# Kernel optimization log

Measured on AMD Instinct MI355X. Metric: run time of the kernel, lower is better.

Reference implementation:

```python
import jax, jax.numpy as jnp
import numpy as np


def setup_inputs() -> dict:
    key = jax.random.key(0)
    ks = jax.random.split(key, 6)
    B, N, D, E, S, H = 4, 4096, 768, 4, 1024, 3072
    sc = lambda d: 1.0 / np.sqrt(d)
    return {
        "x": jax.random.normal(ks[0], (B, N, D), dtype=jnp.float32),
        "phi": jax.random.normal(ks[1], (E, S, D), dtype=jnp.float32) * sc(D),
        "w1": jax.random.normal(ks[2], (E, D, H), dtype=jnp.float32) * sc(D),
        "b1": jnp.zeros((E, H), dtype=jnp.float32),
        "w2": jax.random.normal(ks[3], (E, H, D), dtype=jnp.float32) * sc(H),
        "b2": jnp.zeros((E, D), dtype=jnp.float32),
    }


def reference(x, phi, w1, b1, w2, b2):
    # x: [B,N,D], phi: [E,S,D]
    logits = jnp.einsum('bnd,esd->bnes', x, phi)          # [B,N,E,S]
    B, N, E, S = logits.shape
    dispatch = jax.nn.softmax(logits, axis=1)             # softmax over tokens
    combine = jax.nn.softmax(
        logits.reshape(B, N, E * S), axis=-1
    ).reshape(B, N, E, S)                                 # softmax over all slots
    slots = jnp.einsum('bnd,bnes->besd', x, dispatch)     # [B,E,S,D]
    h = jax.nn.gelu(jnp.einsum('besd,edh->besh', slots, w1) + b1[None, :, None, :])
    y = jnp.einsum('besh,ehd->besd', h, w2) + b2[None, :, None, :]
    out = jnp.einsum('besd,bnes->bnd', y, combine)        # [B,N,D]
    return out
```

## Files before the change

kernel.cpp:

```cpp
#include <hip/hip_runtime.h>
#include <hip/hip_bf16.h>

using u16 = unsigned short;
using short8 = __attribute__((ext_vector_type(8))) short;
using floatx4 = __attribute__((ext_vector_type(4))) float;

#define DEVI static __device__ __forceinline__

constexpr int cB = 4, cN = 4096, cD = 768, cE = 4, cS = 1024, cH = 3072;
constexpr int cES = cE * cS;
constexpr int cHC = cH / 2;

DEVI u16 f2bf(float f) {
  union { float f; unsigned u; } v; v.f = f;
  unsigned r = v.u + 0x7fffu + ((v.u >> 16) & 1u);
  return (u16)(r >> 16);
}
DEVI float bf2f(u16 b) {
  union { unsigned u; float f; } v; v.u = ((unsigned)b) << 16;
  return v.f;
}
DEVI float gelu_tanh(float x) {
  float z = 1.5957691216057308f * (x + 0.044715f * x * x * x);
  z = fminf(fmaxf(z, -30.f), 30.f);
  float e = __expf(z);
  float t = (e - 1.f) / (e + 1.f);
  return 0.5f * x * (1.f + t);
}

DEVI void glds16(const u16* g, u16* l) {
  __builtin_amdgcn_global_load_lds(
      (const __attribute__((address_space(1))) void*)g,
      (__attribute__((address_space(3))) void*)l, 16, 0, 0);
}

__global__ __launch_bounds__(256) void zero_kernel(float* __restrict__ p, int n) {
  int i = blockIdx.x * 256 + threadIdx.x;
  if (i < n) p[i] = 0.f;
}

__global__ __launch_bounds__(256) void convert_kernel(const float* __restrict__ in,
                                                      u16* __restrict__ out, long n) {
  long stride = (long)gridDim.x * 256 * 4;
  for (long idx = ((long)blockIdx.x * 256 + threadIdx.x) * 4; idx < n; idx += stride) {
    float4 v = *(const float4*)(in + idx);
    ushort4 o;
    o.x = f2bf(v.x); o.y = f2bf(v.y); o.z = f2bf(v.z); o.w = f2bf(v.w);
    *(ushort4*)(out + idx) = o;
  }
}

DEVI u16 to_bf(float f) { return f2bf(f); }
DEVI u16 to_bf(u16 u) { return u; }

template <typename Tin>
__global__ __launch_bounds__(256) void transpose_bf16_kernel(const Tin* __restrict__ in,
                                                             u16* __restrict__ out,
                                                             int R, int C,
                                                             long strideIn, long strideOut) {
  __shared__ u16 tile[64][65];
  const Tin* inb = in + (long)blockIdx.z * strideIn;
  u16* outb = out + (long)blockIdx.z * strideOut;
  const int r0 = blockIdx.y * 64, c0 = blockIdx.x * 64;
  const int tid = threadIdx.x;
#pragma unroll
  for (int i = 0; i < 16; i++) {
    int idx = i * 256 + tid;
    int r = idx >> 6, c = idx & 63;
    tile[r][c] = to_bf(inb[(long)(r0 + r) * C + (c0 + c)]);
  }
  __syncthreads();
#pragma unroll
  for (int i = 0; i < 16; i++) {
    int idx = i * 256 + tid;
    int r = idx >> 6, c = idx & 63;
    outb[(long)(c0 + r) * R + (r0 + c)] = tile[c][r];
  }
}

__global__ __launch_bounds__(256) void rowsum_kernel(const u16* __restrict__ P,
                                                     float* __restrict__ Z, int cols) {
  long base = (long)blockIdx.x * cols;
  int tid = threadIdx.x;
  float s = 0.f;
  for (int c = tid * 4; c < cols; c += 256 * 4) {
    ushort4 v = *(const ushort4*)(P + base + c);
    s += bf2f(v.x) + bf2f(v.y) + bf2f(v.z) + bf2f(v.w);
  }
  for (int o = 32; o > 0; o >>= 1) s += __shfl_down(s, o, 64);
  __shared__ float ws4[4];
  if ((tid & 63) == 0) ws4[tid >> 6] = s;
  __syncthreads();
  if (tid == 0) Z[blockIdx.x] = ws4[0] + ws4[1] + ws4[2] + ws4[3];
}

__global__ __launch_bounds__(256) void colsum_kernel(const u16* __restrict__ P,
                                                     float* __restrict__ Z, int cols) {
  int col = blockIdx.x * 256 + threadIdx.x;
  int r0 = blockIdx.y * 256;
  float s = 0.f;
  for (int r = r0; r < r0 + 256; r++) s += bf2f(P[(long)r * cols + col]);
  atomicAdd(Z + col, s);
}

template <int EPI>
__global__ __launch_bounds__(256, 2) void gemm_nt(const u16* __restrict__ A,
                                                  const u16* __restrict__ Bm,
                                                  void* __restrict__ Cout,
                                                  int M, int Nn, int K,
                                                  long ldA, long ldB, long ldC,
                                                  long strideA, long strideB, int modB,
                                                  long strideC,
                                                  const float* __restrict__ epiVec,
                                                  long epiStride, int epiMod) {
  __shared__ u16 lds[4 * 8192];

  const int gx = gridDim.x;
  const int nwg = gx * gridDim.y;
  int flat = blockIdx.y * gx + blockIdx.x;
  if ((nwg & 7) == 0) flat = (flat & 7) * (nwg >> 3) + (flat >> 3);
  const int bxs = flat % gx, bys = flat / gx;

  const int bz = blockIdx.z;
  const u16* Ab = A + (long)bz * strideA;
  const u16* Bb = Bm + (long)(bz % modB) * strideB;
  const float* ev = epiVec + (long)(bz % epiMod) * epiStride;
  const int tileM = bys * 128, tileN = bxs * 128;
  const int tid = threadIdx.x;
  const int wave = tid >> 6, lane = tid & 63;
  const int quad = lane >> 4, l16 = lane & 15;
  const int wm = (wave >> 1) * 64, wn = (wave & 1) * 64;

  const int swzk = (((lane & 3) ^ ((lane >> 3) & 3)) << 3);
  const int r0 = wave * 32 + (lane >> 2);
  const u16* aG0 = Ab + (long)(tileM + r0) * ldA + swzk;
  const u16* aG1 = Ab + (long)(tileM + r0 + 16) * ldA + swzk;
  const u16* bG0 = Bb + (long)(tileN + r0) * ldB + swzk;
  const u16* bG1 = Bb + (long)(tileN + r0 + 16) * ldB + swzk;
  const int ldsW = wave * 1024;

  const int NT = K >> 5;

  auto STAGE = [&](int tt) {
    u16* l = &lds[(tt & 3) * 8192];
    const long ko = (long)tt << 5;
    glds16(aG0 + ko, l + ldsW);
    glds16(aG1 + ko, l + ldsW + 512);
    glds16(bG0 + ko, l + 4096 + ldsW);
    glds16(bG1 + ko, l + 4096 + ldsW + 512);
  };

  floatx4 acc[4][4] = {};
  const int sread = ((quad ^ ((l16 >> 1) & 3)) << 3);

  STAGE(0);
  if (NT > 1) STAGE(1);
  if (NT > 2) STAGE(2);

  for (int t = 0; t < NT; t++) {
    asm volatile("s_barrier" ::: "memory");
    if (t + 3 < NT) STAGE(t + 3);
    const int ahead = NT - 1 - t;
    if (ahead >= 3)      asm volatile("s_waitcnt vmcnt(12)" ::: "memory");
    else if (ahead == 2) asm volatile("s_waitcnt vmcnt(8)" ::: "memory");
    else if (ahead == 1) asm volatile("s_waitcnt vmcnt(4)" ::: "memory");
    else                 asm volatile("s_waitcnt vmcnt(0)" ::: "memory");
    asm volatile("s_barrier" ::: "memory");

    const u16* As = &lds[(t & 3) * 8192];
    const u16* Bs = As + 4096;
    short8 af[4], bq[4];
#pragma unroll
    for (int i = 0; i < 4; i++)
      af[i] = *(const short8*)&As[(wm + i * 16 + l16) * 32 + sread];
#pragma unroll
    for (int j = 0; j < 4; j++)
      bq[j] = *(const short8*)&Bs[(wn + j * 16 + l16) * 32 + sread];
    __builtin_amdgcn_s_setprio(1);
#pragma unroll
    for (int i = 0; i < 4; i++)
#pragma unroll
      for (int j = 0; j < 4; j++)
        acc[i][j] = __builtin_amdgcn_mfma_f32_16x16x32_bf16(af[i], bq[j], acc[i][j], 0, 0, 0);
    __builtin_amdgcn_s_setprio(0);
  }

  const long cBase = (long)bz * strideC;
#pragma unroll
  for (int i = 0; i < 4; i++) {
#pragma unroll
    for (int r = 0; r < 4; r++) {
      const int row = tileM + wm + i * 16 + quad * 4 + r;
      float rscale = 1.f;
      if (EPI == 1 || EPI == 4) rscale = 1.f / ev[row];
#pragma unroll
      for (int j = 0; j < 4; j++) {
        const int col = tileN + wn + j * 16 + l16;
        float v = acc[i][j][r];
        const long cIdx = cBase + (long)row * ldC + col;
        if (EPI == 0) v = __expf(v);
        if (EPI == 1 || EPI == 4) v *= rscale;
        if (EPI == 2) v = gelu_tanh(v + ev[col]);
        if (EPI == 3) v = v + ev[col];
        if (EPI == 5) v = v + bf2f(((u16*)Cout)[cIdx]);
        if (EPI == 4)
          ((float*)Cout)[cIdx] = v;
        else
          ((u16*)Cout)[cIdx] = f2bf(v);
      }
    }
  }
}

template <int EPI>
__global__ __launch_bounds__(512, 2) void gemm256(const u16* __restrict__ A,
                                                  const u16* __restrict__ Bm,
                                                  void* __restrict__ Cout,
                                                  int M, int Nn, int K,
                                                  long ldA, long ldB, long ldC,
                                                  long strideA, long strideB, int modB,
                                                  long strideC,
                                                  const float* __restrict__ epiVec,
                                                  long epiStride, int epiMod) {
  __shared__ u16 lds[2][2][2][8192];

  const int gx = gridDim.x;
  const int nwg = gx * gridDim.y;
  int flat = blockIdx.y * gx + blockIdx.x;
  {
    const int q = nwg >> 3, r = nwg & 7, xc = flat & 7, o = flat >> 3;
    flat = (xc < r ? xc * (q + 1) : r * (q + 1) + (xc - r) * q) + o;
  }
  const int bxs = flat % gx, bys = flat / gx;

  const int bz = blockIdx.z;
  const u16* __restrict__ Ab = A + (long)bz * strideA;
  const u16* __restrict__ Bb = Bm + (long)(bz % modB) * strideB;
  const float* __restrict__ ev = epiVec + (long)(bz % epiMod) * epiStride;
  const int tileM = bys * 256, tileN = bxs * 256;
  const int tid = threadIdx.x;
  const int wave = tid >> 6, lane = tid & 63;
  const int quad = lane >> 4, l16 = lane & 15;
  const int wr = wave >> 2, wc = wave & 3;

  const int kswz = (((lane & 3) ^ ((lane >> 3) & 3)) << 3);
  const int srow = wave * 32 + (lane >> 2);
  const u16* gA = Ab + (long)(tileM + srow) * ldA + kswz;
  const u16* gB = Bb + (long)(tileN + srow) * ldB + kswz;

  const int rdsw = ((quad ^ ((l16 >> 1) & 3)) << 3);
  const int aOff = (wr * 128 + l16) * 32 + rdsw;
  const int bOff = (wc * 64 + l16) * 32 + rdsw;

  const int NT = K >> 6;

#define STA256(buf, kh, tt) do {                                   \
    const u16* _g = gA + ((long)(tt) << 6) + ((kh) << 5);          \
    u16* _l = &lds[buf][0][kh][wave * 1024];                       \
    glds16(_g, _l); glds16(_g + 16 * ldA, _l + 512); } while (0)
#define STB256(buf, kh, tt) do {                                   \
    const u16* _g = gB + ((long)(tt) << 6) + ((kh) << 5);          \
    u16* _l = &lds[buf][1][kh][wave * 1024];                       \
    glds16(_g, _l); glds16(_g + 16 * ldB, _l + 512); } while (0)
#define BAR256 asm volatile("s_barrier" ::: "memory")
#define LGK0   asm volatile("s_waitcnt lgkmcnt(0)" ::: "memory")

  floatx4 acc[8][4] = {};
  short8 af[4], bq[4];

  STA256(0, 0, 0); STB256(0, 0, 0); STA256(0, 1, 0); STB256(0, 1, 0);
  STB256(1, 0, 1); STA256(1, 0, 1); STB256(1, 1, 1);
  asm volatile("s_waitcnt vmcnt(6)" ::: "memory");
  BAR256;

#define TILE256(kt, buf) do {                                                      \
    const bool s1 = (kt) + 1 < NT, s2 = (kt) + 2 < NT;                             \
                                            \
    _Pragma("unroll") for (int i = 0; i < 4; i++)                                  \
      af[i] = *(const short8*)&lds[buf][0][0][aOff + i * 512];                     \
    _Pragma("unroll") for (int n = 0; n < 4; n++)                                  \
      bq[n] = *(const short8*)&lds[buf][1][0][bOff + n * 512];                     \
    if (s1) STA256((buf) ^ 1, 1, (kt) + 1);                                        \
    BAR256; LGK0;                                                                  \
    __builtin_amdgcn_s_setprio(1);                                                 \
    _Pragma("unroll") for (int i = 0; i < 4; i++)                                  \
      _Pragma("unroll") for (int n = 0; n < 4; n++)                                \
        acc[i][n] = __builtin_amdgcn_mfma_f32_16x16x32_bf16(af[i], bq[n], acc[i][n], 0, 0, 0); \
    __builtin_amdgcn_s_setprio(0);                                                 \
    BAR256;                                                                        \
                                         \
    _Pragma("unroll") for (int i = 0; i < 4; i++)                                  \
      af[i] = *(const short8*)&lds[buf][0][0][aOff + (4 + i) * 512];               \
    if (s2) STB256(buf, 0, (kt) + 2);                                              \
    BAR256; LGK0;                                                                  \
    __builtin_amdgcn_s_setprio(1);                                                 \
    _Pragma("unroll") for (int i = 0; i < 4; i++)                                  \
      _Pragma("unroll") for (int n = 0; n < 4; n++)                                \
        acc[4 + i][n] = __builtin_amdgcn_mfma_f32_16x16x32_bf16(af[i], bq[n], acc[4 + i][n], 0, 0, 0); \
    __builtin_amdgcn_s_setprio(0);                                                 \
    BAR256;                                                                        \
                                            \
    _Pragma("unroll") for (int i = 0; i < 4; i++)                                  \
      af[i] = *(const short8*)&lds[buf][0][1][aOff + i * 512];                     \
    _Pragma("unroll") for (int n = 0; n < 4; n++)                                  \
      bq[n] = *(const short8*)&lds[buf][1][1][bOff + n * 512];                     \
    if (s2) STA256(buf, 0, (kt) + 2);                                              \
    BAR256; LGK0;                                                                  \
    __builtin_amdgcn_s_setprio(1);                                                 \
    _Pragma("unroll") for (int i = 0; i < 4; i++)                                  \
      _Pragma("unroll") for (int n = 0; n < 4; n++)                                \
        acc[i][n] = __builtin_amdgcn_mfma_f32_16x16x32_bf16(af[i], bq[n], acc[i][n], 0, 0, 0); \
    __builtin_amdgcn_s_setprio(0);                                                 \
    BAR256;                                                                        \
                                                    \
    _Pragma("unroll") for (int i = 0; i < 4; i++)                                  \
      af[i] = *(const short8*)&lds[buf][0][1][aOff + (4 + i) * 512];               \
    if (s2) STB256(buf, 1, (kt) + 2);                                              \
    BAR256; LGK0;                                                                  \
    __builtin_amdgcn_s_setprio(1);                                                 \
    _Pragma("unroll") for (int i = 0; i < 4; i++)                                  \
      _Pragma("unroll") for (int n = 0; n < 4; n++)                                \
        acc[4 + i][n] = __builtin_amdgcn_mfma_f32_16x16x32_bf16(af[i], bq[n], acc[4 + i][n], 0, 0, 0); \
    __builtin_amdgcn_s_setprio(0);                                                 \
    if (s2)      asm volatile("s_waitcnt vmcnt(6)" ::: "memory");                  \
    else if (s1) asm volatile("s_waitcnt vmcnt(0)" ::: "memory");                  \
    BAR256;                                                                        \
  } while (0)

  for (int kt = 0; kt < NT; kt += 2) {
    TILE256(kt, 0);
    TILE256(kt + 1, 1);
  }
#undef TILE256
#undef STA256
#undef STB256
#undef BAR256
#undef LGK0

  const long cBase = (long)bz * strideC;
#pragma unroll
  for (int m = 0; m < 8; m++) {
#pragma unroll
    for (int r = 0; r < 4; r++) {
      const int row = tileM + wr * 128 + m * 16 + quad * 4 + r;
      float rscale = 1.f;
      if (EPI == 1 || EPI == 4) rscale = 1.f / ev[row];
#pragma unroll
      for (int n = 0; n < 4; n++) {
        const int col = tileN + wc * 64 + n * 16 + l16;
        float v = acc[m][n][r];
        const long cIdx = cBase + (long)row * ldC + col;
        if (EPI == 0) v = __expf(v);
        if (EPI == 1 || EPI == 4) v *= rscale;
        if (EPI == 2) v = gelu_tanh(v + ev[col]);
        if (EPI == 3) v = v + ev[col];
        if (EPI == 5) v = v + bf2f(((u16*)Cout)[cIdx]);
        if (EPI == 4)
          ((float*)Cout)[cIdx] = v;
        else
          ((u16*)Cout)[cIdx] = f2bf(v);
      }
    }
  }
}

extern "C" void kernel_launch(void* const* d_in, const int* in_sizes, int n_in,
                              void* d_out, int out_size, void* d_ws, size_t ws_size,
                              hipStream_t stream) {
  const float* x   = (const float*)d_in[0];
  const float* phi = (const float*)d_in[1];
  const float* w1  = (const float*)d_in[2];
  const float* b1  = (const float*)d_in[3];
  const float* w2  = (const float*)d_in[4];
  const float* b2  = (const float*)d_in[5];
  (void)in_sizes; (void)n_in; (void)out_size; (void)ws_size;
  float* out_f = (float*)d_out;

  char* ws = (char*)d_ws;
  size_t off = 0;
  auto carve = [&](size_t bytes) -> char* {
    char* p = ws + off;
    off += (bytes + 255) & ~(size_t)255;
    return p;
  };

  const size_t SZ_P = (size_t)cN * cES * 2;
  char* R1 = carve(2 * SZ_P);
  u16* Pb  = (u16*)R1;
  u16* Ptb = (u16*)(R1 + SZ_P);
  u16* Hc  = (u16*)R1;
  u16* P2  = (u16*)R1;
  u16* Xbf = (u16*)carve((size_t)cB * cN * cD * 2);
  char* R3 = carve((size_t)cB * cD * cN * 2);
  u16* Xt = (u16*)R3;
  u16* Yv = (u16*)R3;
  char* R4 = carve((size_t)cB * cES * cD * 2);
  u16* Slots = (u16*)R4;
  u16* Yt    = (u16*)R4;
  u16* Phibf = (u16*)carve((size_t)cES * cD * 2);
  u16* W1t = (u16*)carve((size_t)cE * cH * cD * 2);
  u16* W2t = (u16*)carve((size_t)cE * cD * cH * 2);
  float* Z1 = (float*)carve((size_t)cB * cES * 4);
  float* Z2 = (float*)carve((size_t)cB * cN * 4);

  convert_kernel<<<2048, 256, 0, stream>>>(x, Xbf, (long)cB * cN * cD);
  convert_kernel<<<1024, 256, 0, stream>>>(phi, Phibf, (long)cES * cD);
  transpose_bf16_kernel<float><<<dim3(cH / 64, cD / 64, cE), 256, 0, stream>>>(
      w1, W1t, cD, cH, (long)cD * cH, (long)cH * cD);
  transpose_bf16_kernel<float><<<dim3(cD / 64, cH / 64, cE), 256, 0, stream>>>(
      w2, W2t, cH, cD, (long)cH * cD, (long)cD * cH);
  transpose_bf16_kernel<float><<<dim3(cD / 64, cN / 64, cB), 256, 0, stream>>>(
      x, Xt, cN, cD, (long)cN * cD, (long)cD * cN);
  zero_kernel<<<(cB * cES) / 256, 256, 0, stream>>>(Z1, cB * cES);

  for (int b = 0; b < cB; b++) {
    const u16* Xb = Xbf + (long)b * cN * cD;
    gemm256<0><<<dim3(cES / 256, cN / 256, 1), 512, 0, stream>>>(
        Xb, Phibf, Pb, cN, cES, cD, cD, cD, cES,
        0L, 0L, 1, 0L, Z1, 0, 1);
    colsum_kernel<<<dim3(cES / 256, cN / 256, 1), 256, 0, stream>>>(
        Pb, Z1 + (long)b * cES, cES);
    rowsum_kernel<<<cN, 256, 0, stream>>>(Pb, Z2 + (long)b * cN, cES);
    transpose_bf16_kernel<u16><<<dim3(cES / 64, cN / 64, 1), 256, 0, stream>>>(
        Pb, Ptb, cN, cES, 0L, 0L);
    gemm_nt<1><<<dim3(cD / 128, cES / 128, 1), 256, 0, stream>>>(
        Ptb, Xt + (long)b * cD * cN, Slots + (long)b * cES * cD,
        cES, cD, cN, cN, cN, cD,
        0L, 0L, 1, 0L, Z1 + (long)b * cES, 0, 1);
  }

  for (int hc = 0; hc < 2; hc++) {
    const int h0 = hc * cHC;
    gemm256<2><<<dim3(cHC / 256, cS / 256, cB * cE), 512, 0, stream>>>(
        Slots, W1t + (long)h0 * cD, Hc, cS, cHC, cD, cD, cD, cHC,
        (long)cS * cD, (long)cH * cD, cE, (long)cS * cHC, b1 + h0, cH, cE);
    if (hc == 0)
      gemm256<3><<<dim3(cD / 256, cS / 256, cB * cE), 512, 0, stream>>>(
          Hc, W2t + h0, Yv, cS, cD, cHC, cHC, cH, cD,
          (long)cS * cHC, (long)cD * cH, cE, (long)cS * cD, b2, cD, cE);
    else
      gemm256<5><<<dim3(cD / 256, cS / 256, cB * cE), 512, 0, stream>>>(
          Hc, W2t + h0, Yv, cS, cD, cHC, cHC, cH, cD,
          (long)cS * cHC, (long)cD * cH, cE, (long)cS * cD, b2, cD, cE);
  }

  transpose_bf16_kernel<u16><<<dim3(cD / 64, cES / 64, cB), 256, 0, stream>>>(
      Yv, Yt, cES, cD, (long)cES * cD, (long)cD * cES);
  for (int bp = 0; bp < 2; bp++) {
    const u16* Xb = Xbf + (long)(bp * 2) * cN * cD;
    gemm256<0><<<dim3(cES / 256, cN / 256, 2), 512, 0, stream>>>(
        Xb, Phibf, P2, cN, cES, cD, cD, cD, cES,
        (long)cN * cD, 0L, 1, (long)cN * cES, Z1, 0, 1);
    gemm_nt<4><<<dim3(cD / 128, cN / 128, 2), 256, 0, stream>>>(
        P2, Yt + (long)(bp * 2) * cD * cES, out_f + (long)(bp * 2) * cN * cD,
        cN, cD, cES, cES, cES, cD,
        (long)cN * cES, (long)cD * cES, 2, (long)cN * cD,
        Z2 + (long)(bp * 2) * cN, cN, 2);
  }
}
```

Before: 1.169 ms.

## Fuse softmax row/col sums into exp GEMM epilogue and cache exp logits

The exp GEMM epilogue now accumulates row and column sums with wave shuffles and atomics, which removes the separate colsum and rowsum kernels that re-read P. When the workspace is large enough, P is stored for all batches so the second logits GEMM can be skipped. The sums now use f32 values before bf16 rounding. The cache path needs about 306MB of workspace and otherwise falls back to recomputation.

```diff
diff --git a/kernel.cpp b/kernel.cpp
--- a/kernel.cpp
+++ b/kernel.cpp
@@ -76,31 +76,6 @@
     int r = idx >> 6, c = idx & 63;
     outb[(long)(c0 + r) * R + (r0 + c)] = tile[c][r];
   }
-}
-
-__global__ __launch_bounds__(256) void rowsum_kernel(const u16* __restrict__ P,
-                                                     float* __restrict__ Z, int cols) {
-  long base = (long)blockIdx.x * cols;
-  int tid = threadIdx.x;
-  float s = 0.f;
-  for (int c = tid * 4; c < cols; c += 256 * 4) {
-    ushort4 v = *(const ushort4*)(P + base + c);
-    s += bf2f(v.x) + bf2f(v.y) + bf2f(v.z) + bf2f(v.w);
-  }
-  for (int o = 32; o > 0; o >>= 1) s += __shfl_down(s, o, 64);
-  __shared__ float ws4[4];
-  if ((tid & 63) == 0) ws4[tid >> 6] = s;
-  __syncthreads();
-  if (tid == 0) Z[blockIdx.x] = ws4[0] + ws4[1] + ws4[2] + ws4[3];
-}
-
-__global__ __launch_bounds__(256) void colsum_kernel(const u16* __restrict__ P,
-                                                     float* __restrict__ Z, int cols) {
-  int col = blockIdx.x * 256 + threadIdx.x;
-  int r0 = blockIdx.y * 256;
-  float s = 0.f;
-  for (int r = r0; r < r0 + 256; r++) s += bf2f(P[(long)r * cols + col]);
-  atomicAdd(Z + col, s);
 }
 
 template <int EPI>
@@ -221,7 +196,9 @@
                                                   long strideA, long strideB, int modB,
                                                   long strideC,
                                                   const float* __restrict__ epiVec,
-                                                  long epiStride, int epiMod) {
+                                                  long epiStride, int epiMod,
+                                                  float* __restrict__ Zc,
+                                                  float* __restrict__ Zr) {
   __shared__ u16 lds[2][2][2][8192];
 
   const int gx = gridDim.x;
@@ -338,27 +315,59 @@
 #undef LGK0
 
   const long cBase = (long)bz * strideC;
-#pragma unroll
-  for (int m = 0; m < 8; m++) {
-#pragma unroll
-    for (int r = 0; r < 4; r++) {
-      const int row = tileM + wr * 128 + m * 16 + quad * 4 + r;
-      float rscale = 1.f;
-      if (EPI == 1 || EPI == 4) rscale = 1.f / ev[row];
-#pragma unroll
-      for (int n = 0; n < 4; n++) {
-        const int col = tileN + wc * 64 + n * 16 + l16;
-        float v = acc[m][n][r];
-        const long cIdx = cBase + (long)row * ldC + col;
-        if (EPI == 0) v = __expf(v);
-        if (EPI == 1 || EPI == 4) v *= rscale;
-        if (EPI == 2) v = gelu_tanh(v + ev[col]);
-        if (EPI == 3) v = v + ev[col];
-        if (EPI == 5) v = v + bf2f(((u16*)Cout)[cIdx]);
-        if (EPI == 4)
-          ((float*)Cout)[cIdx] = v;
-        else
-          ((u16*)Cout)[cIdx] = f2bf(v);
+  if (EPI == 6) {
+    float csum[4] = {0.f, 0.f, 0.f, 0.f};
+#pragma unroll
+    for (int m = 0; m < 8; m++) {
+#pragma unroll
+      for (int r = 0; r < 4; r++) {
+        const int row = tileM + wr * 128 + m * 16 + quad * 4 + r;
+        float rs = 0.f;
+#pragma unroll
+        for (int n = 0; n < 4; n++) {
+          const int col = tileN + wc * 64 + n * 16 + l16;
+          float v = __expf(acc[m][n][r]);
+          ((u16*)Cout)[cBase + (long)row * ldC + col] = f2bf(v);
+          rs += v;
+          csum[n] += v;
+        }
+        rs += __shfl_xor(rs, 1, 64);
+        rs += __shfl_xor(rs, 2, 64);
+        rs += __shfl_xor(rs, 4, 64);
+        rs += __shfl_xor(rs, 8, 64);
+        if (l16 == 0) atomicAdd(&Zr[row], rs);
+      }
+    }
+#pragma unroll
+    for (int n = 0; n < 4; n++) {
+      float c = csum[n];
+      c += __shfl_xor(c, 16, 64);
+      c += __shfl_xor(c, 32, 64);
+      if (quad == 0) atomicAdd(&Zc[tileN + wc * 64 + n * 16 + l16], c);
+    }
+  } else {
+#pragma unroll
+    for (int m = 0; m < 8; m++) {
+#pragma unroll
+      for (int r = 0; r < 4; r++) {
+        const int row = tileM + wr * 128 + m * 16 + quad * 4 + r;
+        float rscale = 1.f;
+        if (EPI == 1 || EPI == 4) rscale = 1.f / ev[row];
+#pragma unroll
+        for (int n = 0; n < 4; n++) {
+          const int col = tileN + wc * 64 + n * 16 + l16;
+          float v = acc[m][n][r];
+          const long cIdx = cBase + (long)row * ldC + col;
+          if (EPI == 0) v = __expf(v);
+          if (EPI == 1 || EPI == 4) v *= rscale;
+          if (EPI == 2) v = gelu_tanh(v + ev[col]);
+          if (EPI == 3) v = v + ev[col];
+          if (EPI == 5) v = v + bf2f(((u16*)Cout)[cIdx]);
+          if (EPI == 4)
+            ((float*)Cout)[cIdx] = v;
+          else
+            ((u16*)Cout)[cIdx] = f2bf(v);
+        }
       }
     }
   }
@@ -373,7 +382,7 @@
   const float* b1  = (const float*)d_in[3];
   const float* w2  = (const float*)d_in[4];
   const float* b2  = (const float*)d_in[5];
-  (void)in_sizes; (void)n_in; (void)out_size; (void)ws_size;
+  (void)in_sizes; (void)n_in; (void)out_size;
   float* out_f = (float*)d_out;
 
   char* ws = (char*)d_ws;
@@ -384,24 +393,33 @@
     return p;
   };
 
-  const size_t SZ_P = (size_t)cN * cES * 2;
-  char* R1 = carve(2 * SZ_P);
-  u16* Pb  = (u16*)R1;
-  u16* Ptb = (u16*)(R1 + SZ_P);
-  u16* Hc  = (u16*)R1;
-  u16* P2  = (u16*)R1;
+  const size_t SZ_P  = (size_t)cN * cES * 2;
+  const size_t SZ_HC = (size_t)cB * cE * cS * cHC * 2;
+
+  const bool cacheP = ws_size >= (size_t)306 * 1024 * 1024;
+
+  u16 *Pall = nullptr, *PtA = nullptr, *HcA = nullptr;
+  u16 *Pb = nullptr, *Ptb = nullptr, *HcB = nullptr, *P2 = nullptr;
+  if (cacheP) {
+    Pall = (u16*)carve(4 * SZ_P);
+    char* RPH = carve(SZ_HC);
+    PtA = (u16*)RPH; HcA = (u16*)RPH;
+  } else {
+    char* R1 = carve(2 * SZ_P);
+    Pb = (u16*)R1; Ptb = (u16*)(R1 + SZ_P); HcB = (u16*)R1; P2 = (u16*)R1;
+  }
   u16* Xbf = (u16*)carve((size_t)cB * cN * cD * 2);
-  char* R3 = carve((size_t)cB * cD * cN * 2);
-  u16* Xt = (u16*)R3;
-  u16* Yv = (u16*)R3;
-  char* R4 = carve((size_t)cB * cES * cD * 2);
-  u16* Slots = (u16*)R4;
-  u16* Yt    = (u16*)R4;
+  char* R3r = carve((size_t)cB * cD * cN * 2);
+  u16* Xt = (u16*)R3r;
+  u16* Yv = (u16*)R3r;
+  char* R4r = carve((size_t)cB * cES * cD * 2);
+  u16* Slots = (u16*)R4r;
+  u16* Yt    = (u16*)R4r;
   u16* Phibf = (u16*)carve((size_t)cES * cD * 2);
   u16* W1t = (u16*)carve((size_t)cE * cH * cD * 2);
   u16* W2t = (u16*)carve((size_t)cE * cD * cH * 2);
-  float* Z1 = (float*)carve((size_t)cB * cES * 4);
-  float* Z2 = (float*)carve((size_t)cB * cN * 4);
+  float* Z1 = (float*)carve((size_t)(cB * cES + cB * cN) * 4);
+  float* Z2 = Z1 + (size_t)cB * cES;
 
   convert_kernel<<<2048, 256, 0, stream>>>(x, Xbf, (long)cB * cN * cD);
   convert_kernel<<<1024, 256, 0, stream>>>(phi, Phibf, (long)cES * cD);
@@ -411,48 +429,58 @@
       w2, W2t, cH, cD, (long)cH * cD, (long)cD * cH);
   transpose_bf16_kernel<float><<<dim3(cD / 64, cN / 64, cB), 256, 0, stream>>>(
       x, Xt, cN, cD, (long)cN * cD, (long)cD * cN);
-  zero_kernel<<<(cB * cES) / 256, 256, 0, stream>>>(Z1, cB * cES);
+  zero_kernel<<<(cB * (cES + cN)) / 256, 256, 0, stream>>>(Z1, cB * (cES + cN));
 
   for (int b = 0; b < cB; b++) {
     const u16* Xb = Xbf + (long)b * cN * cD;
-    gemm256<0><<<dim3(cES / 256, cN / 256, 1), 512, 0, stream>>>(
-        Xb, Phibf, Pb, cN, cES, cD, cD, cD, cES,
-        0L, 0L, 1, 0L, Z1, 0, 1);
-    colsum_kernel<<<dim3(cES / 256, cN / 256, 1), 256, 0, stream>>>(
-        Pb, Z1 + (long)b * cES, cES);
-    rowsum_kernel<<<cN, 256, 0, stream>>>(Pb, Z2 + (long)b * cN, cES);
+    u16* Pdst = cacheP ? Pall + (size_t)b * cN * cES : Pb;
+    u16* Ptmp = cacheP ? PtA : Ptb;
+    gemm256<6><<<dim3(cES / 256, cN / 256, 1), 512, 0, stream>>>(
+        Xb, Phibf, Pdst, cN, cES, cD, cD, cD, cES,
+        0L, 0L, 1, 0L, Z1, 0, 1,
+        Z1 + (long)b * cES, Z2 + (long)b * cN);
     transpose_bf16_kernel<u16><<<dim3(cES / 64, cN / 64, 1), 256, 0, stream>>>(
-        Pb, Ptb, cN, cES, 0L, 0L);
+        Pdst, Ptmp, cN, cES, 0L, 0L);
     gemm_nt<1><<<dim3(cD / 128, cES / 128, 1), 256, 0, stream>>>(
-        Ptb, Xt + (long)b * cD * cN, Slots + (long)b * cES * cD,
+        Ptmp, Xt + (long)b * cD * cN, Slots + (long)b * cES * cD,
         cES, cD, cN, cN, cN, cD,
         0L, 0L, 1, 0L, Z1 + (long)b * cES, 0, 1);
   }
 
+  u16* Hc = cacheP ? HcA : HcB;
   for (int hc = 0; hc < 2; hc++) {
     const int h0 = hc * cHC;
     gemm256<2><<<dim3(cHC / 256, cS / 256, cB * cE), 512, 0, stream>>>(
         Slots, W1t + (long)h0 * cD, Hc, cS, cHC, cD, cD, cD, cHC,
-        (long)cS * cD, (long)cH * cD, cE, (long)cS * cHC, b1 + h0, cH, cE);
+        (long)cS * cD, (long)cH * cD, cE, (long)cS * cHC, b1 + h0, cH, cE,
+        nullptr, nullptr);
     if (hc == 0)
       gemm256<3><<<dim3(cD / 256, cS / 256, cB * cE), 512, 0, stream>>>(
           Hc, W2t + h0, Yv, cS, cD, cHC, cHC, cH, cD,
-          (long)cS * cHC, (long)cD * cH, cE, (long)cS * cD, b2, cD, cE);
+          (long)cS * cHC, (long)cD * cH, cE, (long)cS * cD, b2, cD, cE,
+          nullptr, nullptr);
     else
       gemm256<5><<<dim3(cD / 256, cS / 256, cB * cE), 512, 0, stream>>>(
           Hc, W2t + h0, Yv, cS, cD, cHC, cHC, cH, cD,
-          (long)cS * cHC, (long)cD * cH, cE, (long)cS * cD, b2, cD, cE);
+          (long)cS * cHC, (long)cD * cH, cE, (long)cS * cD, b2, cD, cE,
+          nullptr, nullptr);
   }
 
   transpose_bf16_kernel<u16><<<dim3(cD / 64, cES / 64, cB), 256, 0, stream>>>(
       Yv, Yt, cES, cD, (long)cES * cD, (long)cD * cES);
   for (int bp = 0; bp < 2; bp++) {
-    const u16* Xb = Xbf + (long)(bp * 2) * cN * cD;
-    gemm256<0><<<dim3(cES / 256, cN / 256, 2), 512, 0, stream>>>(
-        Xb, Phibf, P2, cN, cES, cD, cD, cD, cES,
-        (long)cN * cD, 0L, 1, (long)cN * cES, Z1, 0, 1);
+    const u16* Psrc;
+    if (cacheP) {
+      Psrc = Pall + (size_t)(bp * 2) * cN * cES;
+    } else {
+      const u16* Xb = Xbf + (long)(bp * 2) * cN * cD;
+      gemm256<0><<<dim3(cES / 256, cN / 256, 2), 512, 0, stream>>>(
+          Xb, Phibf, P2, cN, cES, cD, cD, cD, cES,
+          (long)cN * cD, 0L, 1, (long)cN * cES, Z1, 0, 1, nullptr, nullptr);
+      Psrc = P2;
+    }
     gemm_nt<4><<<dim3(cD / 128, cN / 128, 2), 256, 0, stream>>>(
-        P2, Yt + (long)(bp * 2) * cD * cES, out_f + (long)(bp * 2) * cN * cD,
+        Psrc, Yt + (long)(bp * 2) * cD * cES, out_f + (long)(bp * 2) * cN * cD,
         cN, cD, cES, cES, cES, cD,
         (long)cN * cES, (long)cD * cES, 2, (long)cN * cD,
         Z2 + (long)(bp * 2) * cN, cN, 2);
```

New measurement: 1.096 ms. 1.07x faster.
